# Performance work log

Measured on AMD Instinct MI355X. Metric: run time of the kernel, lower is better.

Reference implementation:

```python
import jax, jax.numpy as jnp
import numpy as np

GROUPSIZE = 128

def setup_inputs() -> dict:
    key = jax.random.key(0)
    k1, k2, k3 = jax.random.split(key, 3)
    B, S, K, O = 4, 2048, 4096, 11008
    G = K // GROUPSIZE  # 32 groups
    x = jax.random.normal(k1, (B, S, K), dtype=jnp.float32)
    # int8-valued weight stored as int32 (simulated quantized weights)
    weight = jax.random.randint(k2, (O, K), -128, 128, dtype=jnp.int32)
    # per-(out_channel, group) scales, small positive values
    scales = jax.random.uniform(k3, (O, G), dtype=jnp.float32) * 0.02 + 0.001
    return {"x": x, "weight": weight, "scales": scales}

def reference(x, weight, scales):
    O, K = weight.shape
    G = scales.shape[1]
    gs = K // G
    # groupwise dequant: w_fp[o, g, j] = int8_w[o, g, j] * scales[o, g]
    w_fp = (weight.astype(x.dtype).reshape(O, G, gs) * scales[:, :, None]).reshape(O, K)
    # F.linear: x @ w_fp.T -> [B, S, O]
    return jnp.einsum('bsk,ok->bso', x, w_fp)
```

## Files before the change

### kernel.cpp

```cpp
#include <hip/hip_runtime.h>
#include <hip/hip_bf16.h>

#define MDIM 8192
#define KDIM 4096
#define NDIM 11008
#define GDIM 32

#define BM 256
#define BN 256
#define BK 64
#define NKT (KDIM / BK)
#define MT (MDIM / BM)
#define NT (NDIM / BN)
#define NWG (MT * NT)
#define CPX (NWG / 8)

typedef __attribute__((ext_vector_type(8))) short short8;
typedef __attribute__((ext_vector_type(4))) float f32x4;
typedef __attribute__((address_space(3))) unsigned char lds_u8;

__device__ __forceinline__ unsigned short f2bf(float f) {
    unsigned int u = __float_as_uint(f);
    u += 0x7FFFu + ((u >> 16) & 1u);
    return (unsigned short)(u >> 16);
}

__device__ __forceinline__ void async_ld16(const void* g, lds_u8* l) {
    __builtin_amdgcn_global_load_lds(
        (const __attribute__((address_space(1))) void*)g,
        (__attribute__((address_space(3))) void*)l, 16, 0, 0);
}

__device__ __forceinline__ void stage_half(const unsigned short* src, lds_u8* dst) {
    async_ld16(src, dst);
    async_ld16(src + (size_t)64 * KDIM, dst + 8192);
}

#define BAR()   __builtin_amdgcn_s_barrier()
#define FENCE() asm volatile("" ::: "memory")
#define LGKM0() asm volatile("s_waitcnt lgkmcnt(0)" ::: "memory")
#define LGKM8() asm volatile("s_waitcnt lgkmcnt(8)" ::: "memory")
#define VMW(n)  asm volatile("s_waitcnt vmcnt(" #n ")" ::: "memory")

template<int FB>
__device__ __forceinline__ void ldA4(short8 (&a)[4][2],
                                     const unsigned short* p0,
                                     const unsigned short* p1) {
#pragma unroll
    for (int f = 0; f < 4; ++f) {
        a[f][0] = *(const short8*)(p0 + (FB + f) * 1024);
        a[f][1] = *(const short8*)(p1 + (FB + f) * 1024);
    }
}

template<int NB>
__device__ __forceinline__ void ldB2(short8 (&b)[4][2],
                                     const unsigned short* p0,
                                     const unsigned short* p1) {
#pragma unroll
    for (int n = 0; n < 2; ++n) {
        b[NB + n][0] = *(const short8*)(p0 + (NB + n) * 1024);
        b[NB + n][1] = *(const short8*)(p1 + (NB + n) * 1024);
    }
}

template<int FB, int NB>
__device__ __forceinline__ void mm16(f32x4 (&acc)[8][4],
                                     const short8 (&a)[4][2],
                                     const short8 (&b)[4][2]) {
#pragma unroll
    for (int ks = 0; ks < 2; ++ks)
#pragma unroll
        for (int f = 0; f < 4; ++f)
#pragma unroll
            for (int n = 0; n < 2; ++n)
                acc[FB + f][NB + n] = __builtin_amdgcn_mfma_f32_16x16x32_bf16(
                    a[f][ks], b[NB + n][ks], acc[FB + f][NB + n], 0, 0, 0);
}

__global__ __launch_bounds__(256) void cvt_x_kernel(const float* __restrict__ x,
                                                    unsigned short* __restrict__ xb) {
    size_t i = ((size_t)blockIdx.x * 256 + threadIdx.x) * 8;
    float4 f0 = *(const float4*)(x + i);
    float4 f1 = *(const float4*)(x + i + 4);
    union { unsigned short u[8]; uint4 v; } p;
    p.u[0] = f2bf(f0.x); p.u[1] = f2bf(f0.y); p.u[2] = f2bf(f0.z); p.u[3] = f2bf(f0.w);
    p.u[4] = f2bf(f1.x); p.u[5] = f2bf(f1.y); p.u[6] = f2bf(f1.z); p.u[7] = f2bf(f1.w);
    *(uint4*)(xb + i) = p.v;
}

__global__ __launch_bounds__(256) void deq_w_kernel(const int* __restrict__ w,
                                                    const float* __restrict__ sc,
                                                    unsigned short* __restrict__ wb) {
    size_t idx  = (size_t)blockIdx.x * 256 + threadIdx.x;
    size_t base = idx * 8;
    int o = (int)(base >> 12);
    int k = (int)(base & 4095);
    float s = sc[o * GDIM + (k >> 7)];
    int4 w0 = *(const int4*)(w + base);
    int4 w1 = *(const int4*)(w + base + 4);
    union { unsigned short u[8]; uint4 v; } p;
    p.u[0] = f2bf((float)w0.x * s); p.u[1] = f2bf((float)w0.y * s);
    p.u[2] = f2bf((float)w0.z * s); p.u[3] = f2bf((float)w0.w * s);
    p.u[4] = f2bf((float)w1.x * s); p.u[5] = f2bf((float)w1.y * s);
    p.u[6] = f2bf((float)w1.z * s); p.u[7] = f2bf((float)w1.w * s);
    *(uint4*)(wb + base) = p.v;
}

__global__ __launch_bounds__(512, 2) void gemm256(const unsigned short* __restrict__ A,
                                                  const unsigned short* __restrict__ B,
                                                  float* __restrict__ C) {
    __shared__ unsigned short lds[65536];

    const int tid  = threadIdx.x;
    const int wave = tid >> 6;
    const int lane = tid & 63;
    const int wm = wave >> 2, wn = wave & 3;
    const int q  = lane >> 4;
    const int ml = lane & 15;
    const int s  = ml & 7;

    const int p    = blockIdx.x;
    const int tix  = (p & 7) * CPX + (p >> 3);
    const int bm   = tix & 31;
    const int bn   = tix >> 5;
    const int row0 = bm * BM, col0 = bn * BN;

    const int e0  = ((q    ) ^ s) * 8;
    const int e1  = ((4 + q) ^ s) * 8;
    const int rdA = wm * 8192 + ml * 64;
    const int rdB = 32768 + wn * 4096 + ml * 64;

    const int rA = tid >> 3;
    const int cS = (tid & 7) ^ (rA & 7);
    const unsigned short* gA = A + (size_t)(row0 + rA) * KDIM + cS * 8;
    const unsigned short* gB = B + (size_t)(col0 + rA) * KDIM + cS * 8;
    lds_u8* L8A = (lds_u8*)lds + tid * 16;
    lds_u8* L8B = L8A + 65536;

    stage_half(gA,                      L8A);
    stage_half(gA + (size_t)128 * KDIM, L8A + 16384);
    stage_half(gB,                      L8B);
    stage_half(gB + (size_t)128 * KDIM, L8B + 16384);
    stage_half(gB + 64,                      L8B + 32768);
    stage_half(gB + (size_t)128 * KDIM + 64, L8B + 32768 + 16384);
    const unsigned short* pAg = gA + 64;
    const unsigned short* pBg = gB + 128;
    VMW(4);
    BAR(); FENCE();

    short8 a[4][2], b[4][2];
    f32x4 acc[8][4];
    const f32x4 z = {0.f, 0.f, 0.f, 0.f};
#pragma unroll
    for (int f = 0; f < 8; ++f)
#pragma unroll
        for (int n = 0; n < 4; ++n) acc[f][n] = z;

    for (int kt = 0; kt < NKT; ++kt) {
        const int cur = kt & 1;
        const unsigned short* Lc  = lds + cur * 16384;
        const unsigned short* pA0 = Lc + rdA + e0;
        const unsigned short* pA1 = Lc + rdA + e1;
        const unsigned short* pB0 = Lc + rdB + e0;
        const unsigned short* pB1 = Lc + rdB + e1;
        lds_u8* dA = L8A + (((kt + 1) & 1) << 15);
        lds_u8* dB = L8B + ((cur) << 15);
        const bool stA = (kt + 1 < NKT);
        const bool stB = (kt + 2 < NKT);

        ldA4<0>(a, pA0, pA1);
        ldB2<0>(b, pB0, pB1);
        if (stA) stage_half(pAg, dA);
        LGKM8();
        BAR();
        LGKM0();
        __builtin_amdgcn_s_setprio(1);
        mm16<0, 0>(acc, a, b);
        __builtin_amdgcn_s_setprio(0);
        BAR(); FENCE();

        ldB2<2>(b, pB0, pB1);
        if (stA) stage_half(pAg + (size_t)128 * KDIM, dA + 16384);
        BAR();
        LGKM0();
        __builtin_amdgcn_s_setprio(1);
        mm16<0, 2>(acc, a, b);
        __builtin_amdgcn_s_setprio(0);
        BAR(); FENCE();

        ldA4<4>(a, pA0, pA1);
        if (stB) stage_half(pBg, dB);
        BAR();
        LGKM0();
        __builtin_amdgcn_s_setprio(1);
        mm16<4, 0>(acc, a, b);
        __builtin_amdgcn_s_setprio(0);
        BAR(); FENCE();

        if (stB) stage_half(pBg + (size_t)128 * KDIM, dB + 16384);
        BAR();
        __builtin_amdgcn_s_setprio(1);
        mm16<4, 2>(acc, a, b);
        __builtin_amdgcn_s_setprio(0);
        if (stB)      { VMW(4); }
        else if (stA) { VMW(0); }
        BAR(); FENCE();

        pAg += 64; pBg += 64;
    }

#pragma unroll
    for (int f = 0; f < 8; ++f) {
        const int r0 = row0 + wm * 128 + f * 16 + q * 4;
#pragma unroll
        for (int n = 0; n < 4; ++n) {
            const int c = col0 + wn * 64 + n * 16 + ml;
            float* Cp = C + (size_t)r0 * NDIM + c;
#pragma unroll
            for (int r = 0; r < 4; ++r) Cp[(size_t)r * NDIM] = acc[f][n][r];
        }
    }
}

__global__ __launch_bounds__(256) void gemm_fallback(const float* __restrict__ X,
                                                     const int* __restrict__ W,
                                                     const float* __restrict__ S,
                                                     float* __restrict__ C) {
    int n = blockIdx.x * 256 + threadIdx.x;
    int m = blockIdx.y;
    if (n >= NDIM) return;
    const float* xr = X + (size_t)m * KDIM;
    const int*   wr = W + (size_t)n * KDIM;
    float acc = 0.f;
    for (int g = 0; g < GDIM; ++g) {
        float s = S[n * GDIM + g];
        float part = 0.f;
        for (int k = 0; k < 128; ++k)
            part += xr[g * 128 + k] * (float)wr[g * 128 + k];
        acc += part * s;
    }
    C[(size_t)m * NDIM + n] = acc;
}

extern "C" void kernel_launch(void* const* d_in, const int* in_sizes, int n_in,
                              void* d_out, int out_size, void* d_ws, size_t ws_size,
                              hipStream_t stream) {
    const float* x  = (const float*)d_in[0];
    const int*   w  = (const int*)d_in[1];
    const float* sc = (const float*)d_in[2];
    float* out = (float*)d_out;

    const size_t bytesA = (size_t)MDIM * KDIM * 2;
    const size_t bytesB = (size_t)NDIM * KDIM * 2;

    if (ws_size >= bytesA + bytesB) {
        unsigned short* Abf = (unsigned short*)d_ws;
        unsigned short* Bbf = (unsigned short*)((char*)d_ws + bytesA);

        cvt_x_kernel<<<(MDIM * (size_t)KDIM) / 8 / 256, 256, 0, stream>>>(x, Abf);
        deq_w_kernel<<<(NDIM * (size_t)KDIM) / 8 / 256, 256, 0, stream>>>(w, sc, Bbf);
        gemm256<<<NWG, 512, 0, stream>>>(Abf, Bbf, out);
    } else {
        dim3 grid((NDIM + 255) / 256, MDIM);
        gemm_fallback<<<grid, 256, 0, stream>>>(x, w, sc, out);
    }
}
```

Baseline: 1.192 ms.

## Switch GEMM to 32x32x16 MFMA tiles and merge prep kernels into one launch

The GEMM inner loop moves from 16x16x32 bf16 MFMA to 32x32x16 bf16 MFMA with f32x16 accumulators. The LDS read offsets and swizzle are recomputed, the four-phase schedule is restructured, and the output store mapping is rewritten to match. This is meant to cut LDS read traffic and instruction count per FLOP. Separately, the x-conversion and weight-dequant kernels are fused into a single launch to save one kernel launch and its tail. The risk is in the new register and lgkmcnt wait pattern and in the correctness of the 32x32 output lane mapping.

```diff
diff --git a/kernel.cpp b/kernel.cpp
--- a/kernel.cpp
+++ b/kernel.cpp
@@ -16,7 +16,7 @@
 #define CPX (NWG / 8)
 
 typedef __attribute__((ext_vector_type(8))) short short8;
-typedef __attribute__((ext_vector_type(4))) float f32x4;
+typedef __attribute__((ext_vector_type(16))) float f32x16;
 typedef __attribute__((address_space(3))) unsigned char lds_u8;
 
 __device__ __forceinline__ unsigned short f2bf(float f) {
@@ -39,72 +39,42 @@
 #define BAR()   __builtin_amdgcn_s_barrier()
 #define FENCE() asm volatile("" ::: "memory")
 #define LGKM0() asm volatile("s_waitcnt lgkmcnt(0)" ::: "memory")
+#define LGKM4() asm volatile("s_waitcnt lgkmcnt(4)" ::: "memory")
 #define LGKM8() asm volatile("s_waitcnt lgkmcnt(8)" ::: "memory")
 #define VMW(n)  asm volatile("s_waitcnt vmcnt(" #n ")" ::: "memory")
-
-template<int FB>
-__device__ __forceinline__ void ldA4(short8 (&a)[4][2],
-                                     const unsigned short* p0,
-                                     const unsigned short* p1) {
-#pragma unroll
-    for (int f = 0; f < 4; ++f) {
-        a[f][0] = *(const short8*)(p0 + (FB + f) * 1024);
-        a[f][1] = *(const short8*)(p1 + (FB + f) * 1024);
-    }
-}
-
-template<int NB>
-__device__ __forceinline__ void ldB2(short8 (&b)[4][2],
-                                     const unsigned short* p0,
-                                     const unsigned short* p1) {
-#pragma unroll
-    for (int n = 0; n < 2; ++n) {
-        b[NB + n][0] = *(const short8*)(p0 + (NB + n) * 1024);
-        b[NB + n][1] = *(const short8*)(p1 + (NB + n) * 1024);
-    }
-}
-
-template<int FB, int NB>
-__device__ __forceinline__ void mm16(f32x4 (&acc)[8][4],
-                                     const short8 (&a)[4][2],
-                                     const short8 (&b)[4][2]) {
-#pragma unroll
-    for (int ks = 0; ks < 2; ++ks)
-#pragma unroll
-        for (int f = 0; f < 4; ++f)
-#pragma unroll
-            for (int n = 0; n < 2; ++n)
-                acc[FB + f][NB + n] = __builtin_amdgcn_mfma_f32_16x16x32_bf16(
-                    a[f][ks], b[NB + n][ks], acc[FB + f][NB + n], 0, 0, 0);
-}
-
-__global__ __launch_bounds__(256) void cvt_x_kernel(const float* __restrict__ x,
-                                                    unsigned short* __restrict__ xb) {
-    size_t i = ((size_t)blockIdx.x * 256 + threadIdx.x) * 8;
-    float4 f0 = *(const float4*)(x + i);
-    float4 f1 = *(const float4*)(x + i + 4);
-    union { unsigned short u[8]; uint4 v; } p;
-    p.u[0] = f2bf(f0.x); p.u[1] = f2bf(f0.y); p.u[2] = f2bf(f0.z); p.u[3] = f2bf(f0.w);
-    p.u[4] = f2bf(f1.x); p.u[5] = f2bf(f1.y); p.u[6] = f2bf(f1.z); p.u[7] = f2bf(f1.w);
-    *(uint4*)(xb + i) = p.v;
-}
-
-__global__ __launch_bounds__(256) void deq_w_kernel(const int* __restrict__ w,
-                                                    const float* __restrict__ sc,
-                                                    unsigned short* __restrict__ wb) {
-    size_t idx  = (size_t)blockIdx.x * 256 + threadIdx.x;
-    size_t base = idx * 8;
-    int o = (int)(base >> 12);
-    int k = (int)(base & 4095);
-    float s = sc[o * GDIM + (k >> 7)];
-    int4 w0 = *(const int4*)(w + base);
-    int4 w1 = *(const int4*)(w + base + 4);
-    union { unsigned short u[8]; uint4 v; } p;
-    p.u[0] = f2bf((float)w0.x * s); p.u[1] = f2bf((float)w0.y * s);
-    p.u[2] = f2bf((float)w0.z * s); p.u[3] = f2bf((float)w0.w * s);
-    p.u[4] = f2bf((float)w1.x * s); p.u[5] = f2bf((float)w1.y * s);
-    p.u[6] = f2bf((float)w1.z * s); p.u[7] = f2bf((float)w1.w * s);
-    *(uint4*)(wb + base) = p.v;
+#define SP1()   __builtin_amdgcn_s_setprio(1)
+#define SP0()   __builtin_amdgcn_s_setprio(0)
+
+#define XBLOCKS ((MDIM * (size_t)KDIM) / 8 / 256)
+#define WBLOCKS ((NDIM * (size_t)KDIM) / 8 / 256)
+__global__ __launch_bounds__(256) void prep_kernel(const float* __restrict__ x,
+                                                   const int* __restrict__ w,
+                                                   const float* __restrict__ sc,
+                                                   unsigned short* __restrict__ xb,
+                                                   unsigned short* __restrict__ wb) {
+    size_t b = blockIdx.x;
+    if (b < XBLOCKS) {
+        size_t i = (b * 256 + threadIdx.x) * 8;
+        float4 f0 = *(const float4*)(x + i);
+        float4 f1 = *(const float4*)(x + i + 4);
+        union { unsigned short u[8]; uint4 v; } p;
+        p.u[0] = f2bf(f0.x); p.u[1] = f2bf(f0.y); p.u[2] = f2bf(f0.z); p.u[3] = f2bf(f0.w);
+        p.u[4] = f2bf(f1.x); p.u[5] = f2bf(f1.y); p.u[6] = f2bf(f1.z); p.u[7] = f2bf(f1.w);
+        *(uint4*)(xb + i) = p.v;
+    } else {
+        size_t base = ((b - XBLOCKS) * 256 + threadIdx.x) * 8;
+        int o = (int)(base >> 12);
+        int k = (int)(base & 4095);
+        float s = sc[o * GDIM + (k >> 7)];
+        int4 w0 = *(const int4*)(w + base);
+        int4 w1 = *(const int4*)(w + base + 4);
+        union { unsigned short u[8]; uint4 v; } p;
+        p.u[0] = f2bf((float)w0.x * s); p.u[1] = f2bf((float)w0.y * s);
+        p.u[2] = f2bf((float)w0.z * s); p.u[3] = f2bf((float)w0.w * s);
+        p.u[4] = f2bf((float)w1.x * s); p.u[5] = f2bf((float)w1.y * s);
+        p.u[6] = f2bf((float)w1.z * s); p.u[7] = f2bf((float)w1.w * s);
+        *(uint4*)(wb + base) = p.v;
+    }
 }
 
 __global__ __launch_bounds__(512, 2) void gemm256(const unsigned short* __restrict__ A,
@@ -116,9 +86,9 @@
     const int wave = tid >> 6;
     const int lane = tid & 63;
     const int wm = wave >> 2, wn = wave & 3;
-    const int q  = lane >> 4;
-    const int ml = lane & 15;
-    const int s  = ml & 7;
+    const int l31 = lane & 31;
+    const int hi  = lane >> 5;
+    const int sw  = l31 & 7;
 
     const int p    = blockIdx.x;
     const int tix  = (p & 7) * CPX + (p >> 3);
@@ -126,10 +96,11 @@
     const int bn   = tix >> 5;
     const int row0 = bm * BM, col0 = bn * BN;
 
-    const int e0  = ((q    ) ^ s) * 8;
-    const int e1  = ((4 + q) ^ s) * 8;
-    const int rdA = wm * 8192 + ml * 64;
-    const int rdB = 32768 + wn * 4096 + ml * 64;
+    int eoff[4];
+#pragma unroll
+    for (int ks = 0; ks < 4; ++ks) eoff[ks] = ((2 * ks + hi) ^ sw) * 8;
+    const int rdA = wm * 8192 + l31 * 64;
+    const int rdB = wn * 4096 + l31 * 64;
 
     const int rA = tid >> 3;
     const int cS = (tid & 7) ^ (rA & 7);
@@ -149,60 +120,88 @@
     VMW(4);
     BAR(); FENCE();
 
-    short8 a[4][2], b[4][2];
-    f32x4 acc[8][4];
-    const f32x4 z = {0.f, 0.f, 0.f, 0.f};
-#pragma unroll
-    for (int f = 0; f < 8; ++f)
-#pragma unroll
-        for (int n = 0; n < 4; ++n) acc[f][n] = z;
+    short8 a[2][4], b[2][4];
+    f32x16 acc[4][2];
+#pragma unroll
+    for (int mf = 0; mf < 4; ++mf)
+#pragma unroll
+        for (int nf = 0; nf < 2; ++nf)
+#pragma unroll
+            for (int r = 0; r < 16; ++r) acc[mf][nf][r] = 0.f;
 
     for (int kt = 0; kt < NKT; ++kt) {
         const int cur = kt & 1;
-        const unsigned short* Lc  = lds + cur * 16384;
-        const unsigned short* pA0 = Lc + rdA + e0;
-        const unsigned short* pA1 = Lc + rdA + e1;
-        const unsigned short* pB0 = Lc + rdB + e0;
-        const unsigned short* pB1 = Lc + rdB + e1;
+        const unsigned short* LcA = lds + cur * 16384 + rdA;
+        const unsigned short* LcB = lds + 32768 + cur * 16384 + rdB;
         lds_u8* dA = L8A + (((kt + 1) & 1) << 15);
-        lds_u8* dB = L8B + ((cur) << 15);
+        lds_u8* dB = L8B + (cur << 15);
         const bool stA = (kt + 1 < NKT);
         const bool stB = (kt + 2 < NKT);
 
-        ldA4<0>(a, pA0, pA1);
-        ldB2<0>(b, pB0, pB1);
+#pragma unroll
+        for (int m = 0; m < 2; ++m)
+#pragma unroll
+            for (int ks = 0; ks < 4; ++ks)
+                a[m][ks] = *(const short8*)(LcA + m * 2048 + eoff[ks]);
+#pragma unroll
+        for (int ks = 0; ks < 4; ++ks) b[0][ks] = *(const short8*)(LcB + eoff[ks]);
+#pragma unroll
+        for (int ks = 0; ks < 4; ++ks) b[1][ks] = *(const short8*)(LcB + 2048 + eoff[ks]);
         if (stA) stage_half(pAg, dA);
         LGKM8();
         BAR();
+        LGKM4();
+        SP1();
+#pragma unroll
+        for (int ks = 0; ks < 4; ++ks)
+#pragma unroll
+            for (int m = 0; m < 2; ++m)
+                acc[m][0] = __builtin_amdgcn_mfma_f32_32x32x16_bf16(
+                    a[m][ks], b[0][ks], acc[m][0], 0, 0, 0);
+        SP0();
+        BAR(); FENCE();
+
+        if (stA) stage_half(pAg + (size_t)128 * KDIM, dA + 16384);
+        BAR();
         LGKM0();
-        __builtin_amdgcn_s_setprio(1);
-        mm16<0, 0>(acc, a, b);
-        __builtin_amdgcn_s_setprio(0);
-        BAR(); FENCE();
-
-        ldB2<2>(b, pB0, pB1);
-        if (stA) stage_half(pAg + (size_t)128 * KDIM, dA + 16384);
+        SP1();
+#pragma unroll
+        for (int ks = 0; ks < 4; ++ks)
+#pragma unroll
+            for (int m = 0; m < 2; ++m)
+                acc[m][1] = __builtin_amdgcn_mfma_f32_32x32x16_bf16(
+                    a[m][ks], b[1][ks], acc[m][1], 0, 0, 0);
+        SP0();
+        BAR(); FENCE();
+
+#pragma unroll
+        for (int m = 0; m < 2; ++m)
+#pragma unroll
+            for (int ks = 0; ks < 4; ++ks)
+                a[m][ks] = *(const short8*)(LcA + (2 + m) * 2048 + eoff[ks]);
+        if (stB) stage_half(pBg, dB);
         BAR();
         LGKM0();
-        __builtin_amdgcn_s_setprio(1);
-        mm16<0, 2>(acc, a, b);
-        __builtin_amdgcn_s_setprio(0);
-        BAR(); FENCE();
-
-        ldA4<4>(a, pA0, pA1);
-        if (stB) stage_half(pBg, dB);
-        BAR();
-        LGKM0();
-        __builtin_amdgcn_s_setprio(1);
-        mm16<4, 0>(acc, a, b);
-        __builtin_amdgcn_s_setprio(0);
+        SP1();
+#pragma unroll
+        for (int ks = 0; ks < 4; ++ks)
+#pragma unroll
+            for (int m = 0; m < 2; ++m)
+                acc[2 + m][0] = __builtin_amdgcn_mfma_f32_32x32x16_bf16(
+                    a[m][ks], b[0][ks], acc[2 + m][0], 0, 0, 0);
+        SP0();
         BAR(); FENCE();
 
         if (stB) stage_half(pBg + (size_t)128 * KDIM, dB + 16384);
         BAR();
-        __builtin_amdgcn_s_setprio(1);
-        mm16<4, 2>(acc, a, b);
-        __builtin_amdgcn_s_setprio(0);
+        SP1();
+#pragma unroll
+        for (int ks = 0; ks < 4; ++ks)
+#pragma unroll
+            for (int m = 0; m < 2; ++m)
+                acc[2 + m][1] = __builtin_amdgcn_mfma_f32_32x32x16_bf16(
+                    a[m][ks], b[1][ks], acc[2 + m][1], 0, 0, 0);
+        SP0();
         if (stB)      { VMW(4); }
         else if (stA) { VMW(0); }
         BAR(); FENCE();
@@ -211,14 +210,17 @@
     }
 
 #pragma unroll
-    for (int f = 0; f < 8; ++f) {
-        const int r0 = row0 + wm * 128 + f * 16 + q * 4;
-#pragma unroll
-        for (int n = 0; n < 4; ++n) {
-            const int c = col0 + wn * 64 + n * 16 + ml;
-            float* Cp = C + (size_t)r0 * NDIM + c;
-#pragma unroll
-            for (int r = 0; r < 4; ++r) Cp[(size_t)r * NDIM] = acc[f][n][r];
+    for (int mf = 0; mf < 4; ++mf) {
+        const int rb = row0 + wm * 128 + mf * 32 + 4 * hi;
+#pragma unroll
+        for (int nf = 0; nf < 2; ++nf) {
+            const int c = col0 + wn * 64 + nf * 32 + l31;
+            float* Cp = C + (size_t)rb * NDIM + c;
+#pragma unroll
+            for (int r = 0; r < 16; ++r) {
+                const int dr = (r & 3) + 8 * (r >> 2);
+                Cp[(size_t)dr * NDIM] = acc[mf][nf][r];
+            }
         }
     }
 }
@@ -258,8 +260,7 @@
         unsigned short* Abf = (unsigned short*)d_ws;
         unsigned short* Bbf = (unsigned short*)((char*)d_ws + bytesA);
 
-        cvt_x_kernel<<<(MDIM * (size_t)KDIM) / 8 / 256, 256, 0, stream>>>(x, Abf);
-        deq_w_kernel<<<(NDIM * (size_t)KDIM) / 8 / 256, 256, 0, stream>>>(w, sc, Bbf);
+        prep_kernel<<<(unsigned)(XBLOCKS + WBLOCKS), 256, 0, stream>>>(x, w, sc, Abf, Bbf);
         gemm256<<<NWG, 512, 0, stream>>>(Abf, Bbf, out);
     } else {
         dim3 grid((NDIM + 255) / 256, MDIM);
```

Result: slower. 1.268 ms (+6.3%).
